# Kernel tuning notes

Hardware: AMD Instinct MI355X
Metric: run time of the kernel (lower is better)

## Reference

```python
import jax, jax.numpy as jnp
import numpy as np

B, Q, K = 4, 1024, 1024
QS, KS, H, V = 512, 512, 32, 256


def setup_inputs() -> dict:
    key = jax.random.key(0)
    ks = jax.random.split(key, 6)
    return {
        "queries": jax.random.normal(ks[0], (B, Q, QS), dtype=jnp.float32),
        "keys": jax.random.normal(ks[1], (B, K, KS), dtype=jnp.float32),
        "values": jax.random.normal(ks[2], (B, K, V), dtype=jnp.float32),
        "Wq": jax.random.normal(ks[3], (QS, H), dtype=jnp.float32) / np.sqrt(QS),
        "Wk": jax.random.normal(ks[4], (KS, H), dtype=jnp.float32) / np.sqrt(KS),
        "wv": jax.random.normal(ks[5], (H,), dtype=jnp.float32) / np.sqrt(H),
    }


def reference(queries, keys, values, Wq, Wk, wv):
    # projections
    q = jnp.einsum("bqe,eh->bqh", queries, Wq)  # [B,Q,H]
    k = jnp.einsum("bke,eh->bkh", keys, Wk)     # [B,K,H]
    # additive (Bahdanau) scoring: broadcast add -> tanh -> linear score
    feats = jnp.tanh(q[:, :, None, :] + k[:, None, :, :])  # [B,Q,K,H]
    scores = jnp.einsum("bqkh,h->bqk", feats, wv)           # [B,Q,K]
    attn = jax.nn.softmax(scores, axis=-1)                   # softmax over keys
    # dropout p=0.0 (eval) -> identity
    return jnp.einsum("bqk,bkv->bqv", attn, values)          # [B,Q,V]
```

## Files before the change

### kernel.cpp

```cpp
#include <hip/hip_runtime.h>

#define BATCH 4
#define QDIM 1024
#define KDIM 1024
#define EDIM 512
#define H 32
#define VDIM 256
#define QT 16

#define TWO_LOG2E 2.8853900817779268f
#define LOG2E 1.4426950408889634f

typedef __attribute__((ext_vector_type(8))) short short8;
typedef __attribute__((ext_vector_type(4))) float f32x4;
typedef __attribute__((ext_vector_type(2))) float f32x2;

typedef __attribute__((address_space(3))) void lds_void_t;
typedef __attribute__((address_space(1))) const void gbl_cvoid_t;

static __device__ __forceinline__ void gll16(const void* g, void* l) {
    __builtin_amdgcn_global_load_lds((gbl_cvoid_t*)g, (lds_void_t*)l, 16, 0, 0);
}

static __device__ __forceinline__ unsigned short f32_to_bf16(float f) {
    unsigned int bits = __float_as_uint(f);
    return (unsigned short)((bits + 0x7FFFu + ((bits >> 16) & 1u)) >> 16);
}

static __device__ __forceinline__ unsigned int pack_bf16(float a, float b) {
    unsigned int ua = __float_as_uint(a) + 0x8000u;
    unsigned int ub = __float_as_uint(b) + 0x8000u;
    return __builtin_amdgcn_perm(ub, ua, 0x07060302u);
}

__global__ __launch_bounds__(256) void wprep_kernel(
    const float* __restrict__ Wqm, const float* __restrict__ Wkm,
    unsigned short* __restrict__ wtq, unsigned short* __restrict__ wtk)
{
    const bool is_k = blockIdx.x >= 64;
    const float* W = is_k ? Wkm : Wqm;
    unsigned short* Wt = is_k ? wtk : wtq;
    const int idx = ((int)blockIdx.x & 63) * 256 + (int)threadIdx.x;
    const int e = idx >> 5, c = idx & 31;
    Wt[(size_t)c * EDIM + e] = f32_to_bf16(W[idx]);
}

__global__ __launch_bounds__(256) void prep_kernel(
    const float* __restrict__ qin, const float* __restrict__ kin,
    const unsigned short* __restrict__ wtq, const unsigned short* __restrict__ wtk,
    const float* __restrict__ values,
    float* __restrict__ qp, float* __restrict__ kp,
    unsigned short* __restrict__ vt)
{
    __shared__ float t[64][65];
    __shared__ f32x4 lacc[3][64][2];
    const int tid = (int)threadIdx.x;
    const int bid = (int)blockIdx.x;

    if (bid < 512) {
        const int wave = tid >> 6, lane = tid & 63;
        const bool is_k = bid >= 256;
        const float* X = is_k ? kin : qin;
        const unsigned short* Wt = is_k ? wtk : wtq;
        const int row0 = (bid & 255) * 16;
        const int arow = lane & 15, aq = lane >> 4;
        const int koff = wave * 128 + aq * 8;

        const float* xrow = X + (size_t)(row0 + arow) * EDIM + koff;
        const unsigned short* wt0 = Wt + (size_t)arow * EDIM + koff;
        const unsigned short* wt1 = Wt + (size_t)(arow + 16) * EDIM + koff;

        f32x4 acc0 = {0.f, 0.f, 0.f, 0.f};
        f32x4 acc1 = {0.f, 0.f, 0.f, 0.f};
        #pragma unroll
        for (int s = 0; s < 4; ++s) {
            float4 xa = *reinterpret_cast<const float4*>(xrow + s * 32);
            float4 xb = *reinterpret_cast<const float4*>(xrow + s * 32 + 4);
            unsigned int p0 = pack_bf16(xa.x, xa.y);
            unsigned int p1 = pack_bf16(xa.z, xa.w);
            unsigned int p2 = pack_bf16(xb.x, xb.y);
            unsigned int p3 = pack_bf16(xb.z, xb.w);
            uint4 au = make_uint4(p0, p1, p2, p3);
            short8 af = *reinterpret_cast<const short8*>(&au);
            short8 b0 = *reinterpret_cast<const short8*>(wt0 + s * 32);
            short8 b1 = *reinterpret_cast<const short8*>(wt1 + s * 32);
            acc0 = __builtin_amdgcn_mfma_f32_16x16x32_bf16(af, b0, acc0, 0, 0, 0);
            acc1 = __builtin_amdgcn_mfma_f32_16x16x32_bf16(af, b1, acc1, 0, 0, 0);
        }
        if (wave != 0) {
            lacc[wave - 1][lane][0] = acc0;
            lacc[wave - 1][lane][1] = acc1;
        }
        __syncthreads();
        if (wave == 0) {
            #pragma unroll
            for (int j = 0; j < 3; ++j) {
                acc0 += lacc[j][lane][0];
                acc1 += lacc[j][lane][1];
            }
            if (is_k) {
                #pragma unroll
                for (int r = 0; r < 4; ++r) {
                    const int row = aq * 4 + r;
                    float* orow = kp + (size_t)(row0 + row) * H;
                    orow[arow]      = __builtin_amdgcn_exp2f(acc0[r] * TWO_LOG2E);
                    orow[arow + 16] = __builtin_amdgcn_exp2f(acc1[r] * TWO_LOG2E);
                }
            } else {
                float* tbase = qp + (size_t)(row0 >> 4) * 512;
                #pragma unroll
                for (int r = 0; r < 4; ++r) {
                    const int row = aq * 4 + r;
                    tbase[arow * 16 + row]        = __builtin_amdgcn_exp2f(acc0[r] * TWO_LOG2E);
                    tbase[(arow + 16) * 16 + row] = __builtin_amdgcn_exp2f(acc1[r] * TWO_LOG2E);
                }
            }
        }
    } else {
        const int pid  = bid - 512;
        const int xcd  = pid & 7, slot = pid >> 3;
        const int b    = xcd >> 1;
        const int tnum = slot * 2 + (xcd & 1);
        const int kt = tnum & 15, ct = tnum >> 4;
        const int k0 = kt * 64, c0 = ct * 64;
        const int col4 = (tid & 15) * 4;
        const int krow = tid >> 4;

        #pragma unroll
        for (int i = 0; i < 4; ++i) {
            const int kk = i * 16 + krow;
            float4 v = *reinterpret_cast<const float4*>(
                values + ((size_t)(b * KDIM + k0 + kk) * VDIM + c0 + col4));
            t[kk][col4 + 0] = v.x; t[kk][col4 + 1] = v.y;
            t[kk][col4 + 2] = v.z; t[kk][col4 + 3] = v.w;
        }
        __syncthreads();

        const int col = tid >> 2;
        const int ks  = (tid & 3) * 16;
        unsigned int pk[8];
        #pragma unroll
        for (int j = 0; j < 8; ++j) {
            unsigned int lo = f32_to_bf16(t[ks + 2 * j][col]);
            unsigned int hi = f32_to_bf16(t[ks + 2 * j + 1][col]);
            pk[j] = lo | (hi << 16);
        }
        const int colg = c0 + col;
        const int w_ = colg >> 4, arow_ = colg & 15;
        const int kA = k0 + ks, kB = kA + 8;
        uint4* vt4 = reinterpret_cast<uint4*>(vt);
        const size_t idxA = ((size_t)(b * 16 + w_) * 32 + (kA >> 5)) * 64
                            + ((kA >> 3) & 3) * 16 + arow_;
        const size_t idxB = ((size_t)(b * 16 + w_) * 32 + (kB >> 5)) * 64
                            + ((kB >> 3) & 3) * 16 + arow_;
        vt4[idxA] = make_uint4(pk[0], pk[1], pk[2], pk[3]);
        vt4[idxB] = make_uint4(pk[4], pk[5], pk[6], pk[7]);
    }
}

__global__ __launch_bounds__(1024, 4) void attn_fused(
    const float* __restrict__ qp, const float* __restrict__ kp,
    const unsigned short* __restrict__ vt, const float* __restrict__ wv,
    float* __restrict__ out)
{
    __shared__ __align__(16) unsigned char a_lds[32 * 1024];
    __shared__ __align__(16) unsigned char slab[16 * 4 * 1024];
    __shared__ float inv_lds[QT];

    const int tid = (int)threadIdx.x;
    const int pid = (int)blockIdx.x;
    const int xcd = pid & 7, slot = pid >> 3;
    const int b   = xcd >> 1;
    const int tnum = slot * 2 + (xcd & 1);
    const int q0  = tnum * QT;

    float sumwv = 0.f;
    #pragma unroll
    for (int h = 0; h < H; ++h) sumwv += wv[h];
    const float c0s = sumwv * LOG2E;
    const float c1s = 2.0f * LOG2E;

    {
        const int kk   = tid;
        const int base = (kk >> 5) * 1024 + (kk & 31) * 2;
        float kreg[H];
        const float* krow = kp + (size_t)(b * KDIM + kk) * H;
        #pragma unroll
        for (int i = 0; i < H / 4; ++i) {
            float4 v = *reinterpret_cast<const float4*>(krow + i * 4);
            kreg[i * 4 + 0] = v.x; kreg[i * 4 + 1] = v.y;
            kreg[i * 4 + 2] = v.z; kreg[i * 4 + 3] = v.w;
        }
        const float* eqt = qp + (size_t)((b << 6) | tnum) * 512;

        for (int p = 0; p < 8; ++p) {
            f32x2 s2e = {0.f, 0.f}, s2o = {0.f, 0.f};
            #pragma unroll
            for (int g = 0; g < 8; ++g) {
                const int h = g * 4;
                f32x2 e0 = *reinterpret_cast<const f32x2*>(eqt + (h + 0) * 16 + 2 * p);
                f32x2 e1 = *reinterpret_cast<const f32x2*>(eqt + (h + 1) * 16 + 2 * p);
                f32x2 e2 = *reinterpret_cast<const f32x2*>(eqt + (h + 2) * 16 + 2 * p);
                f32x2 e3 = *reinterpret_cast<const f32x2*>(eqt + (h + 3) * 16 + 2 * p);
                const f32x2 one = {1.f, 1.f};
                f32x2 U0 = e0 * (f32x2){kreg[h + 0], kreg[h + 0]} + one;
                f32x2 U1 = e1 * (f32x2){kreg[h + 1], kreg[h + 1]} + one;
                f32x2 U2 = e2 * (f32x2){kreg[h + 2], kreg[h + 2]} + one;
                f32x2 U3 = e3 * (f32x2){kreg[h + 3], kreg[h + 3]} + one;
                f32x2 n01 = U1 * (f32x2){wv[h + 0], wv[h + 0]}
                          + U0 * (f32x2){wv[h + 1], wv[h + 1]};
                f32x2 n23 = U3 * (f32x2){wv[h + 2], wv[h + 2]}
                          + U2 * (f32x2){wv[h + 3], wv[h + 3]};
                f32x2 d01 = U0 * U1;
                f32x2 d23 = U2 * U3;
                f32x2 n = n01 * d23 + n23 * d01;
                f32x2 d = d01 * d23;
                f32x2 r;
                r.x = __builtin_amdgcn_rcpf(d.x);
                r.y = __builtin_amdgcn_rcpf(d.y);
                if (g & 1) s2o += n * r; else s2e += n * r;
            }
            f32x2 s2 = s2e + s2o;
            float wgtA = __builtin_amdgcn_exp2f(fmaf(-c1s, s2.x, c0s));
            float wgtB = __builtin_amdgcn_exp2f(fmaf(-c1s, s2.y, c0s));
            const int qrA = 2 * p, qrB = 2 * p + 1;
            const int addrA = (base + qrA * 64) ^ ((qrA & 7) << 4);
            const int addrB = (base + qrB * 64) ^ ((qrB & 7) << 4);
            *reinterpret_cast<unsigned short*>(a_lds + addrA) = f32_to_bf16(wgtA);
            *reinterpret_cast<unsigned short*>(a_lds + addrB) = f32_to_bf16(wgtB);
        }
    }
    __syncthreads();

    {
        const int row = tid >> 6;
        const int c   = tid & 63;
        float s = 0.f;
        #pragma unroll
        for (int j = 0; j < 16; ++j) {
            const int k = c + j * 64;
            const int addr = ((k >> 5) * 1024 + row * 64 + (k & 31) * 2)
                             ^ ((row & 7) << 4);
            unsigned int u = *reinterpret_cast<const unsigned short*>(a_lds + addr);
            s += __uint_as_float(u << 16);
        }
        #pragma unroll
        for (int m = 32; m > 0; m >>= 1) s += __shfl_xor(s, m, 64);
        if (c == 0) inv_lds[row] = 1.0f / s;
    }
    __syncthreads();

    const int w    = tid >> 6;
    const int lane = tid & 63;
    const int colb = w * 16;
    const int arow = lane & 15;
    const int aq   = lane >> 4;
    f32x4 acc = {0.f, 0.f, 0.f, 0.f};
    {
        const char* gsrc = reinterpret_cast<const char*>(vt)
                         + ((size_t)(b * 16 + w) * 32) * 1024 + lane * 16;
        char* lbase = reinterpret_cast<char*>(slab) + w * 4096;

        #pragma unroll
        for (int d = 0; d < 3; ++d)
            gll16(gsrc + d * 1024, lbase + d * 1024);

        #pragma unroll 4
        for (int kc = 0; kc < 29; ++kc) {
            gll16(gsrc + (kc + 3) * 1024, lbase + ((kc + 3) & 3) * 1024);
            asm volatile("s_waitcnt vmcnt(3)" ::: "memory");
            const int aaddr = (kc * 1024 + arow * 64 + aq * 16) ^ ((arow & 7) << 4);
            short8 af = *reinterpret_cast<const short8*>(a_lds + aaddr);
            short8 bv = *reinterpret_cast<const short8*>(lbase + (kc & 3) * 1024 + lane * 16);
            acc = __builtin_amdgcn_mfma_f32_16x16x32_bf16(af, bv, acc, 0, 0, 0);
        }
        #define PV_TAIL(KC, VC) { \
            asm volatile("s_waitcnt vmcnt(" #VC ")" ::: "memory"); \
            const int aaddr = ((KC) * 1024 + arow * 64 + aq * 16) ^ ((arow & 7) << 4); \
            short8 af = *reinterpret_cast<const short8*>(a_lds + aaddr); \
            short8 bv = *reinterpret_cast<const short8*>(lbase + ((KC) & 3) * 1024 + lane * 16); \
            acc = __builtin_amdgcn_mfma_f32_16x16x32_bf16(af, bv, acc, 0, 0, 0); }
        PV_TAIL(29, 2)
        PV_TAIL(30, 1)
        PV_TAIL(31, 0)
        #undef PV_TAIL
    }

    __syncthreads();
    {
        float* otile = reinterpret_cast<float*>(a_lds);
        #pragma unroll
        for (int r = 0; r < 4; ++r) {
            const int row = aq * 4 + r;
            otile[row * 264 + colb + arow] = acc[r] * inv_lds[row];
        }
    }
    __syncthreads();
    {
        const float* otile = reinterpret_cast<const float*>(a_lds);
        const int row = tid >> 6;
        const int c4  = (tid & 63) * 4;
        f32x4 v = *reinterpret_cast<const f32x4*>(&otile[row * 264 + c4]);
        *reinterpret_cast<f32x4*>(out + (size_t)(b * QDIM + q0 + row) * VDIM + c4) = v;
    }
}

extern "C" void kernel_launch(void* const* d_in, const int* in_sizes, int n_in,
                              void* d_out, int out_size, void* d_ws, size_t ws_size,
                              hipStream_t stream) {
    const float* queries = (const float*)d_in[0];
    const float* keys    = (const float*)d_in[1];
    const float* values  = (const float*)d_in[2];
    const float* Wq      = (const float*)d_in[3];
    const float* Wk      = (const float*)d_in[4];
    const float* wv      = (const float*)d_in[5];
    float* out = (float*)d_out;

    float* qp = (float*)d_ws;
    float* kp = qp + (size_t)BATCH * QDIM * H;
    unsigned short* vt  = (unsigned short*)(kp + (size_t)BATCH * KDIM * H);
    unsigned short* wtq = vt + (size_t)BATCH * VDIM * KDIM;
    unsigned short* wtk = wtq + (size_t)H * EDIM;

    hipLaunchKernelGGL(wprep_kernel, dim3(128), dim3(256), 0, stream, Wq, Wk, wtq, wtk);
    hipLaunchKernelGGL(prep_kernel, dim3(768), dim3(256), 0, stream,
                       queries, keys, wtq, wtk, values, qp, kp, vt);
    hipLaunchKernelGGL(attn_fused, dim3(BATCH * (QDIM / QT)), dim3(1024), 0, stream,
                       qp, kp, vt, wv, out);
}
```

Measured before the change: 36.78 us.

## Fold weight transpose into prep kernel and stage X tiles through swizzled LDS

Removes the separate wprep kernel launch. Each projection block now loads the full fp32 W matrix itself, converts it to bf16 and transposes it into swizzled LDS. The X rows are staged into LDS with async global_load_lds before the MFMA loop. This saves one launch and its dependency, but every one of 512 blocks now re-reads the 64KB weight matrix, and the 70KB of shared memory may reduce occupancy for the values-transpose blocks.

```diff
diff --git a/kernel.cpp b/kernel.cpp
--- a/kernel.cpp
+++ b/kernel.cpp
@@ -33,27 +33,14 @@
     return __builtin_amdgcn_perm(ub, ua, 0x07060302u);
 }
 
-__global__ __launch_bounds__(256) void wprep_kernel(
-    const float* __restrict__ Wqm, const float* __restrict__ Wkm,
-    unsigned short* __restrict__ wtq, unsigned short* __restrict__ wtk)
-{
-    const bool is_k = blockIdx.x >= 64;
-    const float* W = is_k ? Wkm : Wqm;
-    unsigned short* Wt = is_k ? wtk : wtq;
-    const int idx = ((int)blockIdx.x & 63) * 256 + (int)threadIdx.x;
-    const int e = idx >> 5, c = idx & 31;
-    Wt[(size_t)c * EDIM + e] = f32_to_bf16(W[idx]);
-}
-
 __global__ __launch_bounds__(256) void prep_kernel(
     const float* __restrict__ qin, const float* __restrict__ kin,
-    const unsigned short* __restrict__ wtq, const unsigned short* __restrict__ wtk,
+    const float* __restrict__ Wqm, const float* __restrict__ Wkm,
     const float* __restrict__ values,
     float* __restrict__ qp, float* __restrict__ kp,
     unsigned short* __restrict__ vt)
 {
-    __shared__ float t[64][65];
-    __shared__ f32x4 lacc[3][64][2];
+    __shared__ __align__(16) unsigned char smem[71680];
     const int tid = (int)threadIdx.x;
     const int bid = (int)blockIdx.x;
 
@@ -61,53 +48,92 @@
         const int wave = tid >> 6, lane = tid & 63;
         const bool is_k = bid >= 256;
         const float* X = is_k ? kin : qin;
-        const unsigned short* Wt = is_k ? wtk : wtq;
+        const float* W = is_k ? Wkm : Wqm;
+        float* outp = is_k ? kp : qp;
         const int row0 = (bid & 255) * 16;
         const int arow = lane & 15, aq = lane >> 4;
-        const int koff = wave * 128 + aq * 8;
-
-        const float* xrow = X + (size_t)(row0 + arow) * EDIM + koff;
-        const unsigned short* wt0 = Wt + (size_t)arow * EDIM + koff;
-        const unsigned short* wt1 = Wt + (size_t)(arow + 16) * EDIM + koff;
-
+        const int koff = wave * 128;
+
+        #pragma unroll
+        for (int i = 0; i < 8; ++i) {
+            const int j = wave * 8 + i;
+            const int r = j >> 1, half = j & 1;
+            const int swz = (r & 7) << 4;
+            const char* src = reinterpret_cast<const char*>(X + (size_t)(row0 + r) * EDIM)
+                              + half * 1024 + ((lane * 16) ^ swz);
+            char* dst = reinterpret_cast<char*>(smem) + r * 2048 + half * 1024;
+            gll16(src, dst);
+        }
+
+        {
+            #pragma unroll
+            for (int i = 0; i < 4; ++i) {
+                const int u  = i * 256 + tid;
+                const int eq = u >> 3, hg = u & 7;
+                const int e0 = eq * 4, h4 = hg * 4;
+                float4 w0 = *reinterpret_cast<const float4*>(W + (size_t)(e0 + 0) * H + h4);
+                float4 w1 = *reinterpret_cast<const float4*>(W + (size_t)(e0 + 1) * H + h4);
+                float4 w2 = *reinterpret_cast<const float4*>(W + (size_t)(e0 + 2) * H + h4);
+                float4 w3 = *reinterpret_cast<const float4*>(W + (size_t)(e0 + 3) * H + h4);
+                #define WTROW(HC, C0, C1, C2, C3) { \
+                    const int h = h4 + (HC); \
+                    const int addr = 32 * 1024 + h * 1024 + ((e0 * 2) ^ ((h & 7) << 4)); \
+                    uint2 pk; pk.x = pack_bf16(C0, C1); pk.y = pack_bf16(C2, C3); \
+                    *reinterpret_cast<uint2*>(smem + addr) = pk; }
+                WTROW(0, w0.x, w1.x, w2.x, w3.x)
+                WTROW(1, w0.y, w1.y, w2.y, w3.y)
+                WTROW(2, w0.z, w1.z, w2.z, w3.z)
+                WTROW(3, w0.w, w1.w, w2.w, w3.w)
+                #undef WTROW
+            }
+        }
+        __syncthreads();
+
+        const int swzr = (arow & 7) << 4;
         f32x4 acc0 = {0.f, 0.f, 0.f, 0.f};
         f32x4 acc1 = {0.f, 0.f, 0.f, 0.f};
         #pragma unroll
         for (int s = 0; s < 4; ++s) {
-            float4 xa = *reinterpret_cast<const float4*>(xrow + s * 32);
-            float4 xb = *reinterpret_cast<const float4*>(xrow + s * 32 + 4);
+            const int c = koff + aq * 8 + s * 32;
+            const int A = c * 4;
+            float4 xa = *reinterpret_cast<const float4*>(smem + arow * 2048 + (A ^ swzr));
+            float4 xb = *reinterpret_cast<const float4*>(smem + arow * 2048 + ((A + 16) ^ swzr));
             unsigned int p0 = pack_bf16(xa.x, xa.y);
             unsigned int p1 = pack_bf16(xa.z, xa.w);
             unsigned int p2 = pack_bf16(xb.x, xb.y);
             unsigned int p3 = pack_bf16(xb.z, xb.w);
             uint4 au = make_uint4(p0, p1, p2, p3);
             short8 af = *reinterpret_cast<const short8*>(&au);
-            short8 b0 = *reinterpret_cast<const short8*>(wt0 + s * 32);
-            short8 b1 = *reinterpret_cast<const short8*>(wt1 + s * 32);
+            short8 b0 = *reinterpret_cast<const short8*>(
+                smem + 32 * 1024 + arow * 1024 + ((c * 2) ^ swzr));
+            short8 b1 = *reinterpret_cast<const short8*>(
+                smem + 32 * 1024 + (arow + 16) * 1024 + ((c * 2) ^ swzr));
             acc0 = __builtin_amdgcn_mfma_f32_16x16x32_bf16(af, b0, acc0, 0, 0, 0);
             acc1 = __builtin_amdgcn_mfma_f32_16x16x32_bf16(af, b1, acc1, 0, 0, 0);
         }
+
+        f32x4* lacc = reinterpret_cast<f32x4*>(smem + 64 * 1024);
         if (wave != 0) {
-            lacc[wave - 1][lane][0] = acc0;
-            lacc[wave - 1][lane][1] = acc1;
+            lacc[((wave - 1) * 64 + lane) * 2 + 0] = acc0;
+            lacc[((wave - 1) * 64 + lane) * 2 + 1] = acc1;
         }
         __syncthreads();
         if (wave == 0) {
             #pragma unroll
             for (int j = 0; j < 3; ++j) {
-                acc0 += lacc[j][lane][0];
-                acc1 += lacc[j][lane][1];
+                acc0 += lacc[(j * 64 + lane) * 2 + 0];
+                acc1 += lacc[(j * 64 + lane) * 2 + 1];
             }
             if (is_k) {
                 #pragma unroll
                 for (int r = 0; r < 4; ++r) {
                     const int row = aq * 4 + r;
-                    float* orow = kp + (size_t)(row0 + row) * H;
+                    float* orow = outp + (size_t)(row0 + row) * H;
                     orow[arow]      = __builtin_amdgcn_exp2f(acc0[r] * TWO_LOG2E);
                     orow[arow + 16] = __builtin_amdgcn_exp2f(acc1[r] * TWO_LOG2E);
                 }
             } else {
-                float* tbase = qp + (size_t)(row0 >> 4) * 512;
+                float* tbase = outp + (size_t)(row0 >> 4) * 512;
                 #pragma unroll
                 for (int r = 0; r < 4; ++r) {
                     const int row = aq * 4 + r;
@@ -117,6 +143,7 @@
             }
         }
     } else {
+        float* t = reinterpret_cast<float*>(smem);
         const int pid  = bid - 512;
         const int xcd  = pid & 7, slot = pid >> 3;
         const int b    = xcd >> 1;
@@ -131,8 +158,8 @@
             const int kk = i * 16 + krow;
             float4 v = *reinterpret_cast<const float4*>(
                 values + ((size_t)(b * KDIM + k0 + kk) * VDIM + c0 + col4));
-            t[kk][col4 + 0] = v.x; t[kk][col4 + 1] = v.y;
-            t[kk][col4 + 2] = v.z; t[kk][col4 + 3] = v.w;
+            t[kk * 65 + col4 + 0] = v.x; t[kk * 65 + col4 + 1] = v.y;
+            t[kk * 65 + col4 + 2] = v.z; t[kk * 65 + col4 + 3] = v.w;
         }
         __syncthreads();
 
@@ -141,8 +168,8 @@
         unsigned int pk[8];
         #pragma unroll
         for (int j = 0; j < 8; ++j) {
-            unsigned int lo = f32_to_bf16(t[ks + 2 * j][col]);
-            unsigned int hi = f32_to_bf16(t[ks + 2 * j + 1][col]);
+            unsigned int lo = f32_to_bf16(t[(ks + 2 * j) * 65 + col]);
+            unsigned int hi = f32_to_bf16(t[(ks + 2 * j + 1) * 65 + col]);
             pk[j] = lo | (hi << 16);
         }
         const int colg = c0 + col;
@@ -318,13 +345,10 @@
 
     float* qp = (float*)d_ws;
     float* kp = qp + (size_t)BATCH * QDIM * H;
-    unsigned short* vt  = (unsigned short*)(kp + (size_t)BATCH * KDIM * H);
-    unsigned short* wtq = vt + (size_t)BATCH * VDIM * KDIM;
-    unsigned short* wtk = wtq + (size_t)H * EDIM;
-
-    hipLaunchKernelGGL(wprep_kernel, dim3(128), dim3(256), 0, stream, Wq, Wk, wtq, wtk);
+    unsigned short* vt = (unsigned short*)(kp + (size_t)BATCH * KDIM * H);
+
     hipLaunchKernelGGL(prep_kernel, dim3(768), dim3(256), 0, stream,
-                       queries, keys, wtq, wtk, values, qp, kp, vt);
+                       queries, keys, Wq, Wk, values, qp, kp, vt);
     hipLaunchKernelGGL(attn_fused, dim3(BATCH * (QDIM / QT)), dim3(1024), 0, stream,
                        qp, kp, vt, wv, out);
 }
```

Measured after the change: 31.57 us, median of 2. -14.2%, faster.
